# Optimization experiments

Measured on AMD Instinct MI355X. Metric: run time of the kernel, lower is better.

Reference implementation:

```python
import jax, jax.numpy as jnp
import numpy as np

N, LC, LQ, D = 16, 2048, 256, 256  # D = 2 * LSTM_HIDDEN_DIM


def setup_inputs() -> dict:
    key = jax.random.key(0)
    k1, k2, k3 = jax.random.split(key, 3)
    emb_context = jax.random.normal(k1, (N, LC, D), dtype=jnp.float32)
    emb_query = jax.random.normal(k2, (N, LQ, D), dtype=jnp.float32)
    # Linear(6H=3D, 1, bias=False) weight, flattened to (3D,)
    W = jax.random.normal(k3, (3 * D,), dtype=jnp.float32) / np.sqrt(3 * D)
    return {"emb_context": emb_context, "emb_query": emb_query, "W": W}


def reference(emb_context, emb_query, W):
    d = emb_context.shape[-1]
    # Algebraic decomposition of the expand+cat+linear similarity score:
    # S[n,i,j] = c_i . w_c + q_j . w_q + sum_d c_i[d]*q_j[d]*w_m[d]
    w_c, w_q, w_m = W[:d], W[d:2 * d], W[2 * d:]
    S = (
        jnp.einsum('ncd,d->nc', emb_context, w_c)[:, :, None]
        + jnp.einsum('nqd,d->nq', emb_query, w_q)[:, None, :]
        + jnp.einsum('ncd,nqd->ncq', emb_context * w_m, emb_query)
    )  # (N, Lc, Lq)
    # context-to-query attention
    c2q_attn = jnp.einsum('ncq,nqd->ncd', jax.nn.softmax(S, axis=-1), emb_query)
    # query-to-context attention (max over query dim, softmax over context dim)
    b = jax.nn.softmax(jnp.max(S, axis=2), axis=-1)  # (N, Lc)
    q2c_attn = jnp.einsum('nc,ncd->nd', b, emb_context)[:, None, :]  # (N, 1, D), broadcasts over Lc
    G = jnp.concatenate(
        [emb_context, c2q_attn, emb_context * c2q_attn, emb_context * q2c_attn],
        axis=2,
    )  # (N, Lc, 4D) == (N, Lc, 8*LSTM_HIDDEN_DIM)
    return G
```

## Files before the change

kernel.cpp:

```cpp
#include <hip/hip_runtime.h>
#include <math.h>

#define BN 16
#define LC 2048
#define LQ 256
#define DD 256
#define BM 128
#define NT 512

typedef _Float16 half8 __attribute__((ext_vector_type(8)));
typedef float f32x16 __attribute__((ext_vector_type(16)));
typedef float f32x4 __attribute__((ext_vector_type(4)));

typedef const __attribute__((address_space(1))) void* gas_p;
typedef __attribute__((address_space(3))) void* lds_p;
#define GLOAD_LDS16(gp, lp) \
    __builtin_amdgcn_global_load_lds((gas_p)(gp), (lds_p)(lp), 16, 0, 0)

__device__ __forceinline__ float waveReduceSum(float v) {
#pragma unroll
    for (int o = 32; o > 0; o >>= 1) v += __shfl_xor(v, o, 64);
    return v;
}
__device__ __forceinline__ float waveReduceMax(float v) {
#pragma unroll
    for (int o = 32; o > 0; o >>= 1) v = fmaxf(v, __shfl_xor(v, o, 64));
    return v;
}

__global__ __launch_bounds__(256) void k_prep(const float* __restrict__ q,
                                              const float* __restrict__ W,
                                              _Float16* __restrict__ Qh,
                                              _Float16* __restrict__ QTh,
                                              float* __restrict__ cq) {
    __shared__ float tile[32][257];
    const int n = blockIdx.y;
    const int q0 = blockIdx.x * 32;
    const int t = threadIdx.x;

#pragma unroll
    for (int i = 0; i < 32; ++i) {
        const float v = q[((size_t)(n * LQ + q0 + i)) * DD + t];
        Qh[((size_t)(n * LQ + q0 + i)) * DD + t] = (_Float16)v;
        tile[i][t] = v;
    }
    __syncthreads();

    {
        const int row = t >> 3, sub = t & 7;
        float s = 0.f;
#pragma unroll
        for (int j = 0; j < 32; ++j)
            s = fmaf(tile[row][sub * 32 + j], W[DD + sub * 32 + j], s);
        s += __shfl_xor(s, 1, 64);
        s += __shfl_xor(s, 2, 64);
        s += __shfl_xor(s, 4, 64);
        if (sub == 0) cq[n * LQ + q0 + row] = s;
    }

    const int tx = t & 31, ty = t >> 5;
#pragma unroll
    for (int db = 0; db < 8; ++db) {
#pragma unroll
        for (int i = 0; i < 4; ++i) {
            const int d = db * 32 + ty + 8 * i;
            QTh[((size_t)(n * DD + d)) * LQ + q0 + tx] = (_Float16)tile[tx][d];
        }
    }
}

__global__ __launch_bounds__(NT) void k_main(const float* __restrict__ ctx,
                                             const _Float16* __restrict__ Qh,
                                             const _Float16* __restrict__ QTh,
                                             const float* __restrict__ cq,
                                             const float* __restrict__ W,
                                             float* __restrict__ out,
                                             float* __restrict__ pq,
                                             float* __restrict__ KS) {
    __shared__ _Float16 Abuf[BM * 256];
    __shared__ _Float16 Bbuf[2][256 * 64];
    __shared__ float rowterm[BM];
    __shared__ float m_lds[BM];
    __shared__ float linv_lds[BM];
    __shared__ float eexp[BM];
    __shared__ float redmax[4][BM];
    __shared__ float redsum[4][BM];

    const int t = threadIdx.x;
    const int lane = t & 63, wid = t >> 6;
    const int l31 = lane & 31, lh = lane >> 5;
    const int wr = wid >> 2, wc = wid & 3;
    const int bx = blockIdx.x;
    const int blk = (bx & 7) * 32 + (bx >> 3);
    const int n = blk >> 4;
    const int blk16 = blk & 15;
    const int c0 = blk16 * BM;

    const _Float16* Qhn = Qh + (size_t)n * LQ * DD;
    const _Float16* QThn = QTh + (size_t)n * DD * LQ;

    auto stageB = [&](int kc, const _Float16* src, int buf) {
#pragma unroll
        for (int j = 0; j < 4; ++j) {
            const int r = wid * 32 + j * 8 + (lane >> 3);
            const int gs = (lane & 7) ^ (r & 7);
            const _Float16* gp = src + (size_t)r * 256 + kc * 64 + gs * 8;
            _Float16* lp = &Bbuf[buf][(wid * 32 + j * 8) * 64];
            GLOAD_LDS16(gp, lp);
        }
    };

    auto gemmChunk = [&](f32x16 (&acc)[2][2], int kcA, int buf) {
#pragma unroll
        for (int kk = 0; kk < 4; ++kk) {
            half8 af[2], bf[2];
#pragma unroll
            for (int mt = 0; mt < 2; ++mt) {
                const int row = 64 * wr + 32 * mt + l31;
                const int kb = kcA * 128 + 32 * kk + 16 * lh;
                af[mt] = *(const half8*)((const char*)Abuf + row * 512 + (kb ^ ((row & 7) << 4)));
            }
#pragma unroll
            for (int nt = 0; nt < 2; ++nt) {
                const int row = 64 * wc + 32 * nt + l31;
                const int kb = 32 * kk + 16 * lh;
                bf[nt] = *(const half8*)((const char*)Bbuf[buf] + row * 128 + (kb ^ ((row & 7) << 4)));
            }
#pragma unroll
            for (int mt = 0; mt < 2; ++mt)
#pragma unroll
                for (int nt = 0; nt < 2; ++nt)
                    acc[mt][nt] = __builtin_amdgcn_mfma_f32_32x32x16_f16(af[mt], bf[nt], acc[mt][nt], 0, 0, 0);
        }
    };

    stageB(0, Qhn, 0);

    {
        const int g = t & 31;
        const int r0 = t >> 5;
        float wmv[8], wcv[8];
#pragma unroll
        for (int j = 0; j < 8; ++j) {
            wmv[j] = W[2 * DD + g * 8 + j];
            wcv[j] = W[g * 8 + j];
        }
#pragma unroll
        for (int i = 0; i < 8; ++i) {
            const int r = r0 + 16 * i;
            const float* srcr = ctx + ((size_t)(n * LC + c0 + r)) * DD + g * 8;
            const float4 aa = *(const float4*)srcr;
            const float4 bb = *(const float4*)(srcr + 4);
            const float vals[8] = {aa.x, aa.y, aa.z, aa.w, bb.x, bb.y, bb.z, bb.w};
            half8 cmv;
            float rt = 0.f;
#pragma unroll
            for (int j = 0; j < 8; ++j) {
                cmv[j] = (_Float16)(vals[j] * wmv[j]);
                rt = fmaf(vals[j], wcv[j], rt);
            }
            *(half8*)((char*)Abuf + r * 512 + ((g * 16) ^ ((r & 7) << 4))) = cmv;
#pragma unroll
            for (int o = 16; o > 0; o >>= 1) rt += __shfl_xor(rt, o, 64);
            if (g == 0) rowterm[r] = rt;
        }
    }
    __syncthreads();

    f32x16 acc[2][2] = {};
#pragma unroll
    for (int kc = 0; kc < 4; ++kc) {
        if (kc) __syncthreads();
        if (kc < 3) stageB(kc + 1, Qhn, (kc + 1) & 1);
        else stageB(0, QThn, 0);
        gemmChunk(acc, kc, kc & 1);
    }
    __syncthreads();

    float cqv[2];
    cqv[0] = cq[n * LQ + 64 * wc + l31];
    cqv[1] = cq[n * LQ + 64 * wc + 32 + l31];

#pragma unroll
    for (int mt = 0; mt < 2; ++mt) {
#pragma unroll
        for (int r = 0; r < 16; ++r) {
            const int rl = 64 * wr + 32 * mt + (r & 3) + 8 * (r >> 2) + 4 * lh;
            const float rterm = rowterm[rl];
            const float v0 = acc[mt][0][r] + rterm + cqv[0];
            const float v1 = acc[mt][1][r] + rterm + cqv[1];
            acc[mt][0][r] = v0;
            acc[mt][1][r] = v1;
            float mx = fmaxf(v0, v1);
#pragma unroll
            for (int o = 16; o > 0; o >>= 1) mx = fmaxf(mx, __shfl_xor(mx, o, 64));
            if (l31 == 0) redmax[wc][rl] = mx;
        }
    }
    __syncthreads();
    if (t < BM)
        m_lds[t] = fmaxf(fmaxf(redmax[0][t], redmax[1][t]), fmaxf(redmax[2][t], redmax[3][t]));
    __syncthreads();

    if (t < BM) {
        const float mv = m_lds[t];
        const float kb = waveReduceMax(mv);
        const float e = __expf(mv - kb);
        eexp[t] = e;
        const float sb = waveReduceSum(e);
        if (lane == 0) {
            KS[(n * 32 + blk16 * 2 + (t >> 6)) * 2 + 0] = kb;
            KS[(n * 32 + blk16 * 2 + (t >> 6)) * 2 + 1] = sb;
        }
    }

#pragma unroll
    for (int mt = 0; mt < 2; ++mt) {
#pragma unroll
        for (int r = 0; r < 16; ++r) {
            const int rl = 64 * wr + 32 * mt + (r & 3) + 8 * (r >> 2) + 4 * lh;
            const float mrow = m_lds[rl];
            const float p0 = __expf(acc[mt][0][r] - mrow);
            const float p1 = __expf(acc[mt][1][r] - mrow);
            const int q0 = 64 * wc + l31, q1 = q0 + 32;
            *((_Float16*)((char*)Abuf + rl * 512 + ((q0 * 2) ^ ((rl & 7) << 4)))) = (_Float16)p0;
            *((_Float16*)((char*)Abuf + rl * 512 + ((q1 * 2) ^ ((rl & 7) << 4)))) = (_Float16)p1;
            float sm = p0 + p1;
#pragma unroll
            for (int o = 16; o > 0; o >>= 1) sm += __shfl_xor(sm, o, 64);
            if (l31 == 0) redsum[wc][rl] = sm;
        }
    }
    __syncthreads();
    if (t < BM)
        linv_lds[t] = 1.0f / (redsum[0][t] + redsum[1][t] + redsum[2][t] + redsum[3][t]);
    __syncthreads();

    f32x16 acc2[2][2] = {};
#pragma unroll
    for (int kc = 0; kc < 4; ++kc) {
        if (kc) __syncthreads();
        if (kc < 3) stageB(kc + 1, QThn, (kc + 1) & 1);
        gemmChunk(acc2, kc, kc & 1);
    }

    float pqa[2] = {0.f, 0.f};
#pragma unroll
    for (int mt = 0; mt < 2; ++mt) {
#pragma unroll
        for (int nt = 0; nt < 2; ++nt) {
            const int col = 64 * wc + 32 * nt + l31;
#pragma unroll
            for (int r = 0; r < 16; ++r) {
                const int rl = 64 * wr + 32 * mt + (r & 3) + 8 * (r >> 2) + 4 * lh;
                const size_t gc = (size_t)(n * LC + c0 + rl);
                const float li = linv_lds[rl];
                const float cv = ctx[gc * DD + col];
                const float ov = acc2[mt][nt][r] * li;
                const size_t ob = gc * 1024 + col;
                __builtin_nontemporal_store(cv, &out[ob]);
                __builtin_nontemporal_store(ov, &out[ob + 256]);
                __builtin_nontemporal_store(cv * ov, &out[ob + 512]);
                pqa[nt] = fmaf(eexp[rl], cv, pqa[nt]);
            }
        }
    }
#pragma unroll
    for (int nt = 0; nt < 2; ++nt) {
        pqa[nt] += __shfl_xor(pqa[nt], 32, 64);
        if (lh == 0) {
            const int col = 64 * wc + 32 * nt + l31;
            pq[((size_t)(n * 32 + blk16 * 2 + wr)) * 256 + col] = pqa[nt];
        }
    }
}

__global__ __launch_bounds__(256) void k_tail(const float* __restrict__ ctx,
                                              const float* __restrict__ pq,
                                              const float* __restrict__ KS,
                                              float* __restrict__ out) {
    const int bx = blockIdx.x;
    const int blk = (bx & 7) * 64 + (bx >> 3);
    const int n = blk >> 5;
    const int c0 = (blk & 31) * 64;
    const int t = threadIdx.x;
    const int cg = t & 63;
    const int rs = t >> 6;

    float bmax = -1e30f;
#pragma unroll
    for (int b = 0; b < 32; ++b) bmax = fmaxf(bmax, KS[(n * 32 + b) * 2]);
    float Z = 0.f;
    float4 a = {0.f, 0.f, 0.f, 0.f};
#pragma unroll
    for (int b = 0; b < 32; ++b) {
        const float w = __expf(KS[(n * 32 + b) * 2] - bmax);
        Z = fmaf(w, KS[(n * 32 + b) * 2 + 1], Z);
        const float4 p4 = *(const float4*)&pq[((size_t)(n * 32 + b)) * 256 + cg * 4];
        a.x = fmaf(w, p4.x, a.x);
        a.y = fmaf(w, p4.y, a.y);
        a.z = fmaf(w, p4.z, a.z);
        a.w = fmaf(w, p4.w, a.w);
    }
    const float zi = 1.0f / Z;
    const float4 q2c4 = {a.x * zi, a.y * zi, a.z * zi, a.w * zi};

#pragma unroll
    for (int r = 0; r < 16; ++r) {
        const size_t gc = (size_t)(n * LC + c0 + rs * 16 + r);
        const float4 cv = *(const float4*)&ctx[gc * DD + cg * 4];
        f32x4 ov;
        ov.x = cv.x * q2c4.x;
        ov.y = cv.y * q2c4.y;
        ov.z = cv.z * q2c4.z;
        ov.w = cv.w * q2c4.w;
        __builtin_nontemporal_store(ov, (f32x4*)&out[gc * 1024 + 768 + cg * 4]);
    }
}

extern "C" void kernel_launch(void* const* d_in, const int* in_sizes, int n_in,
                              void* d_out, int out_size, void* d_ws, size_t ws_size,
                              hipStream_t stream) {
    const float* ctx = (const float*)d_in[0];
    const float* q = (const float*)d_in[1];
    const float* W = (const float*)d_in[2];
    float* out = (float*)d_out;

    _Float16* Qh = (_Float16*)d_ws;
    _Float16* QTh = Qh + (size_t)BN * LQ * DD;
    float* fws = (float*)(QTh + (size_t)BN * DD * LQ);
    float* cq = fws;
    float* pq = cq + BN * LQ;
    float* KS = pq + BN * 32 * 256;

    k_prep<<<dim3(LQ / 32, BN), 256, 0, stream>>>(q, W, Qh, QTh, cq);
    k_main<<<BN * LC / BM, NT, 0, stream>>>(ctx, Qh, QTh, cq, W, out, pq, KS);
    k_tail<<<BN * LC / 64, 256, 0, stream>>>(ctx, pq, KS, out);
}
```

Measured before the change: 68.11 us.

## Halve main-kernel row tile to 64 rows with 256 threads and 32-wide K chunks

Shrinks the main fused kernel's context tile from 128 to 64 rows and the block from 512 to 256 threads, doubling the grid to 512 blocks. The staged Q chunk narrows from 64 to 32 halves, with a new swizzle pattern and twice as many K-loop iterations and barriers. The goal is smaller LDS per block so more blocks fit per CU and the 256 CUs are better filled. The cost is that each block re-stages the full Q and Q-transpose, so B-operand traffic per output row doubles, and syncs per unit of work increase.

```diff
diff --git a/kernel.cpp b/kernel.cpp
--- a/kernel.cpp
+++ b/kernel.cpp
@@ -5,8 +5,8 @@
 #define LC 2048
 #define LQ 256
 #define DD 256
-#define BM 128
-#define NT 512
+#define BM 64
+#define NT 256
 
 typedef _Float16 half8 __attribute__((ext_vector_type(8)));
 typedef float f32x16 __attribute__((ext_vector_type(16)));
@@ -78,7 +78,7 @@
                                              float* __restrict__ pq,
                                              float* __restrict__ KS) {
     __shared__ _Float16 Abuf[BM * 256];
-    __shared__ _Float16 Bbuf[2][256 * 64];
+    __shared__ _Float16 Bbuf[2][256 * 32];
     __shared__ float rowterm[BM];
     __shared__ float m_lds[BM];
     __shared__ float linv_lds[BM];
@@ -87,14 +87,14 @@
     __shared__ float redsum[4][BM];
 
     const int t = threadIdx.x;
-    const int lane = t & 63, wid = t >> 6;
+    const int lane = t & 63;
     const int l31 = lane & 31, lh = lane >> 5;
-    const int wr = wid >> 2, wc = wid & 3;
+    const int wc = t >> 6;
     const int bx = blockIdx.x;
-    const int blk = (bx & 7) * 32 + (bx >> 3);
-    const int n = blk >> 4;
-    const int blk16 = blk & 15;
-    const int c0 = blk16 * BM;
+    const int blk = (bx & 7) * 64 + (bx >> 3);
+    const int n = blk >> 5;
+    const int blk32 = blk & 31;
+    const int c0 = blk32 * BM;
 
     const _Float16* Qhn = Qh + (size_t)n * LQ * DD;
     const _Float16* QThn = QTh + (size_t)n * DD * LQ;
@@ -102,29 +102,29 @@
     auto stageB = [&](int kc, const _Float16* src, int buf) {
 #pragma unroll
         for (int j = 0; j < 4; ++j) {
-            const int r = wid * 32 + j * 8 + (lane >> 3);
-            const int gs = (lane & 7) ^ (r & 7);
-            const _Float16* gp = src + (size_t)r * 256 + kc * 64 + gs * 8;
-            _Float16* lp = &Bbuf[buf][(wid * 32 + j * 8) * 64];
+            const int r = j * 64 + (t >> 2);
+            const int gs = (t & 3) ^ (r & 3);
+            const _Float16* gp = src + (size_t)r * 256 + kc * 32 + gs * 8;
+            _Float16* lp = &Bbuf[buf][(j * 64 + ((t >> 2) & ~15)) * 32];
             GLOAD_LDS16(gp, lp);
         }
     };
 
     auto gemmChunk = [&](f32x16 (&acc)[2][2], int kcA, int buf) {
 #pragma unroll
-        for (int kk = 0; kk < 4; ++kk) {
+        for (int kk = 0; kk < 2; ++kk) {
             half8 af[2], bf[2];
 #pragma unroll
             for (int mt = 0; mt < 2; ++mt) {
-                const int row = 64 * wr + 32 * mt + l31;
-                const int kb = kcA * 128 + 32 * kk + 16 * lh;
+                const int row = 32 * mt + l31;
+                const int kb = kcA * 64 + 32 * kk + 16 * lh;
                 af[mt] = *(const half8*)((const char*)Abuf + row * 512 + (kb ^ ((row & 7) << 4)));
             }
 #pragma unroll
             for (int nt = 0; nt < 2; ++nt) {
                 const int row = 64 * wc + 32 * nt + l31;
-                const int kb = 32 * kk + 16 * lh;
-                bf[nt] = *(const half8*)((const char*)Bbuf[buf] + row * 128 + (kb ^ ((row & 7) << 4)));
+                const int g = 2 * kk + lh;
+                bf[nt] = *(const half8*)((const char*)Bbuf[buf] + row * 64 + ((g ^ (row & 3)) * 16));
             }
 #pragma unroll
             for (int mt = 0; mt < 2; ++mt)
@@ -147,7 +147,7 @@
         }
 #pragma unroll
         for (int i = 0; i < 8; ++i) {
-            const int r = r0 + 16 * i;
+            const int r = r0 + 8 * i;
             const float* srcr = ctx + ((size_t)(n * LC + c0 + r)) * DD + g * 8;
             const float4 aa = *(const float4*)srcr;
             const float4 bb = *(const float4*)(srcr + 4);
@@ -169,9 +169,9 @@
 
     f32x16 acc[2][2] = {};
 #pragma unroll
-    for (int kc = 0; kc < 4; ++kc) {
+    for (int kc = 0; kc < 8; ++kc) {
         if (kc) __syncthreads();
-        if (kc < 3) stageB(kc + 1, Qhn, (kc + 1) & 1);
+        if (kc < 7) stageB(kc + 1, Qhn, (kc + 1) & 1);
         else stageB(0, QThn, 0);
         gemmChunk(acc, kc, kc & 1);
     }
@@ -185,7 +185,7 @@
     for (int mt = 0; mt < 2; ++mt) {
 #pragma unroll
         for (int r = 0; r < 16; ++r) {
-            const int rl = 64 * wr + 32 * mt + (r & 3) + 8 * (r >> 2) + 4 * lh;
+            const int rl = 32 * mt + (r & 3) + 8 * (r >> 2) + 4 * lh;
             const float rterm = rowterm[rl];
             const float v0 = acc[mt][0][r] + rterm + cqv[0];
             const float v1 = acc[mt][1][r] + rterm + cqv[1];
@@ -208,9 +208,9 @@
         const float e = __expf(mv - kb);
         eexp[t] = e;
         const float sb = waveReduceSum(e);
-        if (lane == 0) {
-            KS[(n * 32 + blk16 * 2 + (t >> 6)) * 2 + 0] = kb;
-            KS[(n * 32 + blk16 * 2 + (t >> 6)) * 2 + 1] = sb;
+        if (t == 0) {
+            KS[(n * 32 + blk32) * 2 + 0] = kb;
+            KS[(n * 32 + blk32) * 2 + 1] = sb;
         }
     }
 
@@ -218,7 +218,7 @@
     for (int mt = 0; mt < 2; ++mt) {
 #pragma unroll
         for (int r = 0; r < 16; ++r) {
-            const int rl = 64 * wr + 32 * mt + (r & 3) + 8 * (r >> 2) + 4 * lh;
+            const int rl = 32 * mt + (r & 3) + 8 * (r >> 2) + 4 * lh;
             const float mrow = m_lds[rl];
             const float p0 = __expf(acc[mt][0][r] - mrow);
             const float p1 = __expf(acc[mt][1][r] - mrow);
@@ -238,9 +238,9 @@
 
     f32x16 acc2[2][2] = {};
 #pragma unroll
-    for (int kc = 0; kc < 4; ++kc) {
+    for (int kc = 0; kc < 8; ++kc) {
         if (kc) __syncthreads();
-        if (kc < 3) stageB(kc + 1, QThn, (kc + 1) & 1);
+        if (kc < 7) stageB(kc + 1, QThn, (kc + 1) & 1);
         gemmChunk(acc2, kc, kc & 1);
     }
 
@@ -252,7 +252,7 @@
             const int col = 64 * wc + 32 * nt + l31;
 #pragma unroll
             for (int r = 0; r < 16; ++r) {
-                const int rl = 64 * wr + 32 * mt + (r & 3) + 8 * (r >> 2) + 4 * lh;
+                const int rl = 32 * mt + (r & 3) + 8 * (r >> 2) + 4 * lh;
                 const size_t gc = (size_t)(n * LC + c0 + rl);
                 const float li = linv_lds[rl];
                 const float cv = ctx[gc * DD + col];
@@ -270,7 +270,7 @@
         pqa[nt] += __shfl_xor(pqa[nt], 32, 64);
         if (lh == 0) {
             const int col = 64 * wc + 32 * nt + l31;
-            pq[((size_t)(n * 32 + blk16 * 2 + wr)) * 256 + col] = pqa[nt];
+            pq[((size_t)(n * 32 + blk32)) * 256 + col] = pqa[nt];
         }
     }
 }
```

Result: slower. 71.81 us (+5.4%).

## Give each wave its own query-column slice to replace block barriers with vmcnt waits

Applied to the files above, without the earlier changes.

Changes the k_main wave layout from a 2x4 grid of 64x64 tiles to eight waves that each own 32 query columns across all 128 context rows. Each wave stages only its own slice of Q/Q^T into LDS, so the per-chunk __syncthreads can become a wave-local s_waitcnt vmcnt(0). Partial softmax statistics are now produced per block instead of per half-block, so k_tail and the workspace shrink from 32 to 16 partials per batch. In exchange, each wave reads twice as many A fragments from LDS, and the next chunk's load is now issued after the current GEMM chunk, which leaves less load/compute overlap.

```diff
diff --git a/kernel.cpp b/kernel.cpp
--- a/kernel.cpp
+++ b/kernel.cpp
@@ -16,6 +16,9 @@
 typedef __attribute__((address_space(3))) void* lds_p;
 #define GLOAD_LDS16(gp, lp) \
     __builtin_amdgcn_global_load_lds((gas_p)(gp), (lds_p)(lp), 16, 0, 0)
+
+#define WAIT_VM0() do { asm volatile("s_waitcnt vmcnt(0)" ::: "memory"); \
+                        __builtin_amdgcn_sched_barrier(0); } while (0)
 
 __device__ __forceinline__ float waveReduceSum(float v) {
 #pragma unroll
@@ -78,63 +81,60 @@
                                              float* __restrict__ pq,
                                              float* __restrict__ KS) {
     __shared__ _Float16 Abuf[BM * 256];
-    __shared__ _Float16 Bbuf[2][256 * 64];
+    __shared__ _Float16 Bbuf[2][8][32 * 64];
     __shared__ float rowterm[BM];
     __shared__ float m_lds[BM];
     __shared__ float linv_lds[BM];
     __shared__ float eexp[BM];
-    __shared__ float redmax[4][BM];
-    __shared__ float redsum[4][BM];
+    __shared__ float redmax[8][BM];
+    __shared__ float redsum[8][BM];
 
     const int t = threadIdx.x;
-    const int lane = t & 63, wid = t >> 6;
+    const int lane = t & 63, w = t >> 6;
     const int l31 = lane & 31, lh = lane >> 5;
-    const int wr = wid >> 2, wc = wid & 3;
     const int bx = blockIdx.x;
     const int blk = (bx & 7) * 32 + (bx >> 3);
     const int n = blk >> 4;
     const int blk16 = blk & 15;
     const int c0 = blk16 * BM;
+    const int col = 32 * w + l31;
 
     const _Float16* Qhn = Qh + (size_t)n * LQ * DD;
     const _Float16* QThn = QTh + (size_t)n * DD * LQ;
 
-    auto stageB = [&](int kc, const _Float16* src, int buf) {
+    auto stageW = [&](int kc, const _Float16* src, int buf) {
 #pragma unroll
         for (int j = 0; j < 4; ++j) {
-            const int r = wid * 32 + j * 8 + (lane >> 3);
-            const int gs = (lane & 7) ^ (r & 7);
-            const _Float16* gp = src + (size_t)r * 256 + kc * 64 + gs * 8;
-            _Float16* lp = &Bbuf[buf][(wid * 32 + j * 8) * 64];
+            const int rl = j * 8 + (lane >> 3);
+            const int gs = (lane & 7) ^ (rl & 7);
+            const _Float16* gp = src + (size_t)(32 * w + rl) * 256 + kc * 64 + gs * 8;
+            _Float16* lp = &Bbuf[buf][w][j * 8 * 64];
             GLOAD_LDS16(gp, lp);
         }
     };
 
-    auto gemmChunk = [&](f32x16 (&acc)[2][2], int kcA, int buf) {
+    auto gemmChunk = [&](f32x16 (&acc)[4], int kcA, int buf) {
 #pragma unroll
         for (int kk = 0; kk < 4; ++kk) {
-            half8 af[2], bf[2];
-#pragma unroll
-            for (int mt = 0; mt < 2; ++mt) {
-                const int row = 64 * wr + 32 * mt + l31;
+            half8 af[4], bf;
+            {
+                const int rlb = l31;
+                const int kb = 32 * kk + 16 * lh;
+                bf = *(const half8*)((const char*)&Bbuf[buf][w][0] + rlb * 128 + (kb ^ ((rlb & 7) << 4)));
+            }
+#pragma unroll
+            for (int mt = 0; mt < 4; ++mt) {
+                const int row = 32 * mt + l31;
                 const int kb = kcA * 128 + 32 * kk + 16 * lh;
                 af[mt] = *(const half8*)((const char*)Abuf + row * 512 + (kb ^ ((row & 7) << 4)));
             }
 #pragma unroll
-            for (int nt = 0; nt < 2; ++nt) {
-                const int row = 64 * wc + 32 * nt + l31;
-                const int kb = 32 * kk + 16 * lh;
-                bf[nt] = *(const half8*)((const char*)Bbuf[buf] + row * 128 + (kb ^ ((row & 7) << 4)));
-            }
-#pragma unroll
-            for (int mt = 0; mt < 2; ++mt)
-#pragma unroll
-                for (int nt = 0; nt < 2; ++nt)
-                    acc[mt][nt] = __builtin_amdgcn_mfma_f32_32x32x16_f16(af[mt], bf[nt], acc[mt][nt], 0, 0, 0);
+            for (int mt = 0; mt < 4; ++mt)
+                acc[mt] = __builtin_amdgcn_mfma_f32_32x32x16_f16(af[mt], bf, acc[mt], 0, 0, 0);
         }
     };
 
-    stageB(0, Qhn, 0);
+    stageW(0, Qhn, 0);
 
     {
         const int g = t & 31;
@@ -167,112 +167,102 @@
     }
     __syncthreads();
 
-    f32x16 acc[2][2] = {};
+    f32x16 acc[4] = {};
 #pragma unroll
     for (int kc = 0; kc < 4; ++kc) {
-        if (kc) __syncthreads();
-        if (kc < 3) stageB(kc + 1, Qhn, (kc + 1) & 1);
-        else stageB(0, QThn, 0);
+        if (kc) WAIT_VM0();
         gemmChunk(acc, kc, kc & 1);
-    }
-    __syncthreads();
-
-    float cqv[2];
-    cqv[0] = cq[n * LQ + 64 * wc + l31];
-    cqv[1] = cq[n * LQ + 64 * wc + 32 + l31];
-
-#pragma unroll
-    for (int mt = 0; mt < 2; ++mt) {
+        if (kc < 3) stageW(kc + 1, Qhn, (kc + 1) & 1);
+        else stageW(0, QThn, 0);
+    }
+
+    const float cqv = cq[n * LQ + col];
+
+#pragma unroll
+    for (int mt = 0; mt < 4; ++mt) {
 #pragma unroll
         for (int r = 0; r < 16; ++r) {
-            const int rl = 64 * wr + 32 * mt + (r & 3) + 8 * (r >> 2) + 4 * lh;
-            const float rterm = rowterm[rl];
-            const float v0 = acc[mt][0][r] + rterm + cqv[0];
-            const float v1 = acc[mt][1][r] + rterm + cqv[1];
-            acc[mt][0][r] = v0;
-            acc[mt][1][r] = v1;
-            float mx = fmaxf(v0, v1);
+            const int rl = 32 * mt + (r & 3) + 8 * (r >> 2) + 4 * lh;
+            const float v0 = acc[mt][r] + rowterm[rl] + cqv;
+            acc[mt][r] = v0;
+            float mx = v0;
 #pragma unroll
             for (int o = 16; o > 0; o >>= 1) mx = fmaxf(mx, __shfl_xor(mx, o, 64));
-            if (l31 == 0) redmax[wc][rl] = mx;
-        }
-    }
-    __syncthreads();
-    if (t < BM)
-        m_lds[t] = fmaxf(fmaxf(redmax[0][t], redmax[1][t]), fmaxf(redmax[2][t], redmax[3][t]));
-    __syncthreads();
-
+            if (l31 == 0) redmax[w][rl] = mx;
+        }
+    }
+    __syncthreads();
     if (t < BM) {
-        const float mv = m_lds[t];
-        const float kb = waveReduceMax(mv);
-        const float e = __expf(mv - kb);
-        eexp[t] = e;
-        const float sb = waveReduceSum(e);
-        if (lane == 0) {
-            KS[(n * 32 + blk16 * 2 + (t >> 6)) * 2 + 0] = kb;
-            KS[(n * 32 + blk16 * 2 + (t >> 6)) * 2 + 1] = sb;
-        }
-    }
-
-#pragma unroll
-    for (int mt = 0; mt < 2; ++mt) {
+        float mv = redmax[0][t];
+#pragma unroll
+        for (int j = 1; j < 8; ++j) mv = fmaxf(mv, redmax[j][t]);
+        m_lds[t] = mv;
+    }
+    __syncthreads();
+
+    if (t < 64) {
+        const float m0 = m_lds[t];
+        const float m1 = m_lds[t + 64];
+        const float kb = waveReduceMax(fmaxf(m0, m1));
+        const float e0 = __expf(m0 - kb);
+        const float e1 = __expf(m1 - kb);
+        eexp[t] = e0;
+        eexp[t + 64] = e1;
+        const float sb = waveReduceSum(e0 + e1);
+        if (t == 0) {
+            KS[(n * 16 + blk16) * 2 + 0] = kb;
+            KS[(n * 16 + blk16) * 2 + 1] = sb;
+        }
+    }
+
+#pragma unroll
+    for (int mt = 0; mt < 4; ++mt) {
 #pragma unroll
         for (int r = 0; r < 16; ++r) {
-            const int rl = 64 * wr + 32 * mt + (r & 3) + 8 * (r >> 2) + 4 * lh;
-            const float mrow = m_lds[rl];
-            const float p0 = __expf(acc[mt][0][r] - mrow);
-            const float p1 = __expf(acc[mt][1][r] - mrow);
-            const int q0 = 64 * wc + l31, q1 = q0 + 32;
-            *((_Float16*)((char*)Abuf + rl * 512 + ((q0 * 2) ^ ((rl & 7) << 4)))) = (_Float16)p0;
-            *((_Float16*)((char*)Abuf + rl * 512 + ((q1 * 2) ^ ((rl & 7) << 4)))) = (_Float16)p1;
-            float sm = p0 + p1;
+            const int rl = 32 * mt + (r & 3) + 8 * (r >> 2) + 4 * lh;
+            const float p0 = __expf(acc[mt][r] - m_lds[rl]);
+            *((_Float16*)((char*)Abuf + rl * 512 + ((col * 2) ^ ((rl & 7) << 4)))) = (_Float16)p0;
+            float sm = p0;
 #pragma unroll
             for (int o = 16; o > 0; o >>= 1) sm += __shfl_xor(sm, o, 64);
-            if (l31 == 0) redsum[wc][rl] = sm;
-        }
-    }
-    __syncthreads();
-    if (t < BM)
-        linv_lds[t] = 1.0f / (redsum[0][t] + redsum[1][t] + redsum[2][t] + redsum[3][t]);
-    __syncthreads();
-
-    f32x16 acc2[2][2] = {};
+            if (l31 == 0) redsum[w][rl] = sm;
+        }
+    }
+    __syncthreads();
+    if (t < BM) {
+        float s8 = redsum[0][t];
+#pragma unroll
+        for (int j = 1; j < 8; ++j) s8 += redsum[j][t];
+        linv_lds[t] = 1.0f / s8;
+    }
+    __syncthreads();
+
+    f32x16 acc2[4] = {};
 #pragma unroll
     for (int kc = 0; kc < 4; ++kc) {
-        if (kc) __syncthreads();
-        if (kc < 3) stageB(kc + 1, QThn, (kc + 1) & 1);
+        if (kc) WAIT_VM0();
         gemmChunk(acc2, kc, kc & 1);
-    }
-
-    float pqa[2] = {0.f, 0.f};
-#pragma unroll
-    for (int mt = 0; mt < 2; ++mt) {
-#pragma unroll
-        for (int nt = 0; nt < 2; ++nt) {
-            const int col = 64 * wc + 32 * nt + l31;
-#pragma unroll
-            for (int r = 0; r < 16; ++r) {
-                const int rl = 64 * wr + 32 * mt + (r & 3) + 8 * (r >> 2) + 4 * lh;
-                const size_t gc = (size_t)(n * LC + c0 + rl);
-                const float li = linv_lds[rl];
-                const float cv = ctx[gc * DD + col];
-                const float ov = acc2[mt][nt][r] * li;
-                const size_t ob = gc * 1024 + col;
-                __builtin_nontemporal_store(cv, &out[ob]);
-                __builtin_nontemporal_store(ov, &out[ob + 256]);
-                __builtin_nontemporal_store(cv * ov, &out[ob + 512]);
-                pqa[nt] = fmaf(eexp[rl], cv, pqa[nt]);
-            }
-        }
-    }
-#pragma unroll
-    for (int nt = 0; nt < 2; ++nt) {
-        pqa[nt] += __shfl_xor(pqa[nt], 32, 64);
-        if (lh == 0) {
-            const int col = 64 * wc + 32 * nt + l31;
-            pq[((size_t)(n * 32 + blk16 * 2 + wr)) * 256 + col] = pqa[nt];
-        }
-    }
+        if (kc < 3) stageW(kc + 1, QThn, (kc + 1) & 1);
+    }
+
+    float pqa = 0.f;
+#pragma unroll
+    for (int mt = 0; mt < 4; ++mt) {
+#pragma unroll
+        for (int r = 0; r < 16; ++r) {
+            const int rl = 32 * mt + (r & 3) + 8 * (r >> 2) + 4 * lh;
+            const size_t gc = (size_t)(n * LC + c0 + rl);
+            const float cv = ctx[gc * DD + col];
+            const float ov = acc2[mt][r] * linv_lds[rl];
+            const size_t ob = gc * 1024 + col;
+            __builtin_nontemporal_store(cv, &out[ob]);
+            __builtin_nontemporal_store(ov, &out[ob + 256]);
+            __builtin_nontemporal_store(cv * ov, &out[ob + 512]);
+            pqa = fmaf(eexp[rl], cv, pqa);
+        }
+    }
+    pqa += __shfl_xor(pqa, 32, 64);
+    if (lh == 0) pq[((size_t)(n * 16 + blk16)) * 256 + col] = pqa;
 }
 
 __global__ __launch_bounds__(256) void k_tail(const float* __restrict__ ctx,
@@ -289,18 +279,18 @@
 
     float bmax = -1e30f;
 #pragma unroll
-    for (int b = 0; b < 32; ++b) bmax = fmaxf(bmax, KS[(n * 32 + b) * 2]);
+    for (int b = 0; b < 16; ++b) bmax = fmaxf(bmax, KS[(n * 16 + b) * 2]);
     float Z = 0.f;
     float4 a = {0.f, 0.f, 0.f, 0.f};
 #pragma unroll
-    for (int b = 0; b < 32; ++b) {
-        const float w = __expf(KS[(n * 32 + b) * 2] - bmax);
-        Z = fmaf(w, KS[(n * 32 + b) * 2 + 1], Z);
-        const float4 p4 = *(const float4*)&pq[((size_t)(n * 32 + b)) * 256 + cg * 4];
-        a.x = fmaf(w, p4.x, a.x);
-        a.y = fmaf(w, p4.y, a.y);
-        a.z = fmaf(w, p4.z, a.z);
-        a.w = fmaf(w, p4.w, a.w);
+    for (int b = 0; b < 16; ++b) {
+        const float wv = __expf(KS[(n * 16 + b) * 2] - bmax);
+        Z = fmaf(wv, KS[(n * 16 + b) * 2 + 1], Z);
+        const float4 p4 = *(const float4*)&pq[((size_t)(n * 16 + b)) * 256 + cg * 4];
+        a.x = fmaf(wv, p4.x, a.x);
+        a.y = fmaf(wv, p4.y, a.y);
+        a.z = fmaf(wv, p4.z, a.z);
+        a.w = fmaf(wv, p4.w, a.w);
     }
     const float zi = 1.0f / Z;
     const float4 q2c4 = {a.x * zi, a.y * zi, a.z * zi, a.w * zi};
@@ -331,7 +321,7 @@
     float* fws = (float*)(QTh + (size_t)BN * DD * LQ);
     float* cq = fws;
     float* pq = cq + BN * LQ;
-    float* KS = pq + BN * 32 * 256;
+    float* KS = pq + BN * 16 * 256;
 
     k_prep<<<dim3(LQ / 32, BN), 256, 0, stream>>>(q, W, Qh, QTh, cq);
     k_main<<<BN * LC / BM, NT, 0, stream>>>(ctx, Qh, QTh, cq, W, out, pq, KS);
```

After: 81.34 us. 1.19x slower.
